# Performance work log

Measured on AMD Instinct MI355X. Metric: run time of the kernel, lower is better.

The kernel has to match this reference:

```python
import jax, jax.numpy as jnp
import numpy as np

HIDDEN = 1024
QDIM = 16
B, S = 4, 2048
EPS = 1e-8


def setup_inputs() -> dict:
    key = jax.random.key(0)
    ks = jax.random.split(key, 12)
    sc_h = 1.0 / np.sqrt(HIDDEN)
    inp = {
        "x": jax.random.normal(ks[0], (B, S, HIDDEN), dtype=jnp.float32),
        "Wq": jax.random.normal(ks[1], (HIDDEN, HIDDEN), dtype=jnp.float32) * sc_h,
        "bq": jnp.zeros((HIDDEN,), dtype=jnp.float32),
        "Wk": jax.random.normal(ks[2], (HIDDEN, HIDDEN), dtype=jnp.float32) * sc_h,
        "bk": jnp.zeros((HIDDEN,), dtype=jnp.float32),
        "Wv": jax.random.normal(ks[3], (HIDDEN, HIDDEN), dtype=jnp.float32) * sc_h,
        "bv": jnp.zeros((HIDDEN,), dtype=jnp.float32),
        "We": jax.random.normal(ks[4], (HIDDEN, QDIM), dtype=jnp.float32) * sc_h,
        "be": jnp.zeros((QDIM,), dtype=jnp.float32),
        "Wo": jax.random.normal(ks[5], (HIDDEN, HIDDEN), dtype=jnp.float32) * sc_h,
        "bo": jnp.zeros((HIDDEN,), dtype=jnp.float32),
    }
    return inp


def _quantum_embed(h, We, be):
    # Linear projection to quantum amplitude space, then normalize to a unit state.
    z = h @ We + be                     # [..., QDIM]
    nrm = jnp.sqrt(jnp.sum(z * z, axis=-1, keepdims=True) + EPS)
    return z / nrm


def reference(x, Wq, bq, Wk, bk, Wv, bv, We, be, Wo, bo):
    # Projections
    q = x @ Wq + bq                     # [B,S,H]
    k = x @ Wk + bk
    v = x @ Wv + bv
    # Quantum state embeddings (unit-normalized amplitudes)
    q_q = _quantum_embed(q, We, be)     # [B,S,QDIM]
    k_q = _quantum_embed(k, We, be)
    # Quantum fidelity similarity |<q|k>|^2, vectorized over all pairs
    ov = jnp.einsum("bqd,bkd->bqk", q_q, k_q)   # [B,S,S]
    attn = jax.nn.softmax(ov * ov, axis=-1)
    attended = jnp.einsum("bqk,bkh->bqh", attn, v)
    return attended @ Wo + bo
```

## Files before the change

### kernel.cpp

```cpp
#include <hip/hip_runtime.h>

#define H 1024
#define QD 16
#define BATCH 4
#define SEQ 2048
#define MROWS 8192
#define KCH 64

typedef __bf16 bf16x8 __attribute__((ext_vector_type(8)));
typedef __bf16 bf16x4 __attribute__((ext_vector_type(4)));
typedef float f32x4 __attribute__((ext_vector_type(4)));

__device__ __forceinline__ void async_g2l_16(const void* g, void* l) {
  __builtin_amdgcn_global_load_lds(
      (const __attribute__((address_space(1))) unsigned int*)g,
      (__attribute__((address_space(3))) unsigned int*)l, 16, 0, 0);
}

__global__ __launch_bounds__(256) void cvt_split(const float* __restrict__ src,
                                                 __bf16* __restrict__ hi,
                                                 __bf16* __restrict__ lo, int n) {
  int i = (blockIdx.x * 256 + threadIdx.x) * 4;
  if (i < n) {
    float4 f = *(const float4*)(src + i);
    bf16x4 h, l;
    h[0] = (__bf16)f.x; l[0] = (__bf16)(f.x - (float)h[0]);
    h[1] = (__bf16)f.y; l[1] = (__bf16)(f.y - (float)h[1]);
    h[2] = (__bf16)f.z; l[2] = (__bf16)(f.z - (float)h[2]);
    h[3] = (__bf16)f.w; l[3] = (__bf16)(f.w - (float)h[3]);
    *(bf16x4*)(hi + i) = h;
    *(bf16x4*)(lo + i) = l;
  }
}

__global__ __launch_bounds__(256) void transpose_cvt_f32_bf16(
    const float* __restrict__ src, __bf16* __restrict__ dst, int R, int C) {
  __shared__ float t[32][33];
  const int rb = blockIdx.y * 32, cb = blockIdx.x * 32;
  const int c = threadIdx.x & 31;
  const int r0 = threadIdx.x >> 5;
#pragma unroll
  for (int rr = r0; rr < 32; rr += 8)
    t[rr][c] = src[(long)(rb + rr) * C + cb + c];
  __syncthreads();
#pragma unroll
  for (int rr = r0; rr < 32; rr += 8)
    dst[(long)(cb + rr) * R + rb + c] = (__bf16)t[c][rr];
}

__global__ __launch_bounds__(256) void k2_cqk(const float* __restrict__ Wq,
                                              const float* __restrict__ Wk,
                                              const float* __restrict__ We,
                                              __bf16* __restrict__ Cth,
                                              __bf16* __restrict__ Ctl) {
  const int gw = blockIdx.x * 4 + (threadIdx.x >> 6);
  const int lane = threadIdx.x & 63;
  const int mat = gw & 1, k = gw >> 1;
  const float* Wrow = (mat ? Wk : Wq) + (long)k * H;
  const int col = lane & 15, q4 = lane >> 4;
  float acc = 0.f;
  for (int n0 = 0; n0 < 256; ++n0) {
    int n = q4 * 256 + n0;
    acc += Wrow[n] * We[n * QD + col];
  }
  acc += __shfl_xor(acc, 16);
  acc += __shfl_xor(acc, 32);
  if (lane < 16) {
    __bf16 hi = (__bf16)acc;
    __bf16 lo = (__bf16)(acc - (float)hi);
    long idx = (long)(mat * 16 + col) * H + k;
    Cth[idx] = hi;
    Ctl[idx] = lo;
  }
}

__global__ void k2b_dvec(const float* __restrict__ bq, const float* __restrict__ bk,
                         const float* __restrict__ We, const float* __restrict__ be,
                         float* __restrict__ dvec) {
  int j = threadIdx.x;
  if (j < 32) {
    int mat = j >> 4, col = j & 15;
    const float* b = mat ? bk : bq;
    float acc = be[col];
    for (int n = 0; n < H; ++n) acc += b[n] * We[n * QD + col];
    dvec[j] = acc;
  }
}

__global__ __launch_bounds__(256) void k3_embed_mfma(
    const __bf16* __restrict__ xh, const __bf16* __restrict__ xl,
    const __bf16* __restrict__ Cth, const __bf16* __restrict__ Ctl,
    const float* __restrict__ dvec, __bf16* __restrict__ qq32,
    __bf16* __restrict__ kk32) {
  __shared__ __bf16 Ah[32 * 64];
  __shared__ __bf16 Al[32 * 64];
  __shared__ __bf16 Bh[32 * 64];
  __shared__ __bf16 Bl[32 * 64];
  const int tid = threadIdx.x;
  const int lane = tid & 63;
  const int w = tid >> 6;
  const int rowhalf = w >> 1;
  const int ntile = w & 1;
  const int l15 = lane & 15, quad = lane >> 4;
  const long rowBase = (long)blockIdx.x * 32;

  const int srow = tid >> 3;
  const int segsw = ((tid & 7) ^ (srow & 7)) * 8;
  const __bf16* agh = xh + (rowBase + srow) * H + segsw;
  const __bf16* agl = xl + (rowBase + srow) * H + segsw;
  const __bf16* bgh = Cth + (long)srow * H + segsw;
  const __bf16* bgl = Ctl + (long)srow * H + segsw;
  __bf16* lah = &Ah[srow * 64 + (tid & 7) * 8];
  __bf16* lal = &Al[srow * 64 + (tid & 7) * 8];
  __bf16* lbh = &Bh[srow * 64 + (tid & 7) * 8];
  __bf16* lbl = &Bl[srow * 64 + (tid & 7) * 8];

  f32x4 acc;
  acc[0] = 0.f; acc[1] = 0.f; acc[2] = 0.f; acc[3] = 0.f;
  const int arow = (rowhalf * 16 + l15) * 64;
  const int brow = (ntile * 16 + l15) * 64;
  const int h7 = l15 & 7;

  for (int k0 = 0; k0 < H; k0 += 64) {
    async_g2l_16(agh + k0, lah);
    async_g2l_16(agl + k0, lal);
    async_g2l_16(bgh + k0, lbh);
    async_g2l_16(bgl + k0, lbl);
    __syncthreads();
#pragma unroll
    for (int s = 0; s < 2; ++s) {
      const int slot = ((s * 4 + quad) ^ h7) * 8;
      bf16x8 fah = *(const bf16x8*)&Ah[arow + slot];
      bf16x8 fal = *(const bf16x8*)&Al[arow + slot];
      bf16x8 fbh = *(const bf16x8*)&Bh[brow + slot];
      bf16x8 fbl = *(const bf16x8*)&Bl[brow + slot];
      acc = __builtin_amdgcn_mfma_f32_16x16x32_bf16(fah, fbh, acc, 0, 0, 0);
      acc = __builtin_amdgcn_mfma_f32_16x16x32_bf16(fal, fbh, acc, 0, 0, 0);
      acc = __builtin_amdgcn_mfma_f32_16x16x32_bf16(fah, fbl, acc, 0, 0, 0);
    }
    __syncthreads();
  }

  const float dv = dvec[ntile * 16 + l15];
  const float osc = ntile ? 1.0f : 1.20112240878f;
  __bf16* outp = ntile ? kk32 : qq32;
#pragma unroll
  for (int r = 0; r < 4; ++r) {
    float z = acc[r] + dv;
    float s2 = z * z;
    s2 += __shfl_xor(s2, 1);
    s2 += __shfl_xor(s2, 2);
    s2 += __shfl_xor(s2, 4);
    s2 += __shfl_xor(s2, 8);
    float val = z * rsqrtf(s2 + 1e-8f) * osc;
    long row = rowBase + rowhalf * 16 + quad * 4 + r;
    outp[row * 32 + l15] = (__bf16)val;
    outp[row * 32 + 16 + l15] = (__bf16)0.f;
  }
}

__global__ __launch_bounds__(512) void fused_attn(
    const __bf16* __restrict__ qq32, const __bf16* __restrict__ kk32,
    const __bf16* __restrict__ v_t, __bf16* __restrict__ attn) {
  __shared__ __bf16 Vlds[3][256 * KCH];
  __shared__ __bf16 Plds[2][128 * KCH];
  __shared__ float rsum2[128 * 2];
  const int tid = threadIdx.x;
  const int lane = tid & 63;
  const int w = tid >> 6;
  const int l15 = lane & 15, quad = lane >> 4;
  const int ws_k = w & 1, ws_q = w >> 1;
  const int wp_h = w & 3, wp_q = w >> 2;
  const int b = blockIdx.z;
  const long qbase = (long)blockIdx.x * 128;
  const long hbase = (long)blockIdx.y * 256;

  bf16x8 bq[2];
  {
    const __bf16* qqp =
        qq32 + ((long)b * SEQ + qbase + ws_q * 32 + l15) * 32 + quad * 8;
    bq[0] = *(const bf16x8*)qqp;
    bq[1] = *(const bf16x8*)(qqp + 16 * 32);
  }
  const __bf16* kkb = kk32 + ((long)b * SEQ + ws_k * 32 + l15) * 32 + quad * 8;

  const int vR = tid >> 3;
  const int vSL = (tid & 7) ^ (vR & 7);
  const __bf16* vgbase = v_t + (long)b * H * SEQ + (hbase + vR) * SEQ + vSL * 8;

  f32x4 acc[4][4];
#pragma unroll
  for (int i = 0; i < 4; ++i)
#pragma unroll
    for (int j = 0; j < 4; ++j) {
      acc[i][j][0] = 0.f; acc[i][j][1] = 0.f; acc[i][j][2] = 0.f; acc[i][j][3] = 0.f;
    }
  float rsPart[2] = {0.f, 0.f};

#pragma unroll
  for (int j = 0; j < 4; ++j)
    async_g2l_16(vgbase + (long)j * 64 * SEQ, &Vlds[0][j * 64 * KCH + tid * 8]);
  bf16x8 ak[2];
  ak[0] = *(const bf16x8*)kkb;
  ak[1] = *(const bf16x8*)(kkb + 16 * 32);

  int vcur = 0, vnxt = 1;
  for (int t = 0; t < SEQ / KCH; ++t) {
    const int kn = ((t + 1) & (SEQ / KCH - 1)) * KCH;
#pragma unroll
    for (int j = 0; j < 4; ++j)
      async_g2l_16(vgbase + (long)j * 64 * SEQ + kn,
                   &Vlds[vnxt][j * 64 * KCH + tid * 8]);

    __bf16* Pw = Plds[t & 1];
#pragma unroll
    for (int i = 0; i < 2; ++i) {
#pragma unroll
      for (int n = 0; n < 2; ++n) {
        f32x4 s;
        s[0] = 0.f; s[1] = 0.f; s[2] = 0.f; s[3] = 0.f;
        s = __builtin_amdgcn_mfma_f32_16x16x32_bf16(ak[i], bq[n], s, 0, 0, 0);
        bf16x4 pw;
        float part = 0.f;
#pragma unroll
        for (int r = 0; r < 4; ++r) {
          float wgt = exp2f(s[r] * s[r]);
          part += wgt;
          pw[r] = (__bf16)wgt;
        }
        rsPart[n] += part;
        const int q = ws_q * 32 + n * 16 + l15;
        const int g = ws_k * 4 + i * 2 + (quad >> 1);
        *(bf16x4*)&Pw[q * KCH + ((g ^ (q & 7)) << 3) + (quad & 1) * 4] = pw;
      }
    }
    ak[0] = *(const bf16x8*)(kkb + (long)kn * 32);
    ak[1] = *(const bf16x8*)(kkb + (long)(kn + 16) * 32);

    asm volatile("s_waitcnt lgkmcnt(0)" ::: "memory");
    asm volatile("s_waitcnt vmcnt(6)" ::: "memory");
    __builtin_amdgcn_sched_barrier(0);
    __builtin_amdgcn_s_barrier();

    const __bf16* Vr = Vlds[vcur];
#pragma unroll
    for (int ks = 0; ks < 2; ++ks) {
      bf16x8 ap[4], bv[4];
#pragma unroll
      for (int i = 0; i < 4; ++i) {
        const int q = wp_q * 64 + i * 16 + l15;
        ap[i] = *(const bf16x8*)&Pw[q * KCH + (((ks * 4 + quad) ^ (q & 7)) << 3)];
      }
#pragma unroll
      for (int j = 0; j < 4; ++j) {
        const int vr = wp_h * 64 + j * 16 + l15;
        bv[j] = *(const bf16x8*)&Vr[vr * KCH + (((ks * 4 + quad) ^ (vr & 7)) << 3)];
      }
#pragma unroll
      for (int i = 0; i < 4; ++i)
#pragma unroll
        for (int j = 0; j < 4; ++j)
          acc[i][j] =
              __builtin_amdgcn_mfma_f32_16x16x32_bf16(ap[i], bv[j], acc[i][j], 0, 0, 0);
    }
    const int third = 3 - vcur - vnxt;
    vcur = vnxt;
    vnxt = third;
  }

#pragma unroll
  for (int n = 0; n < 2; ++n) {
    float vs = rsPart[n];
    vs += __shfl_xor(vs, 16);
    vs += __shfl_xor(vs, 32);
    if (lane < 16) rsum2[(ws_q * 32 + n * 16 + l15) * 2 + ws_k] = vs;
  }
  __syncthreads();

  float rinv[4][4];
#pragma unroll
  for (int i = 0; i < 4; ++i)
#pragma unroll
    for (int r = 0; r < 4; ++r) {
      int row = wp_q * 64 + i * 16 + quad * 4 + r;
      rinv[i][r] = 1.0f / (rsum2[row * 2] + rsum2[row * 2 + 1]);
    }

  __bf16* ob = attn + ((long)b * SEQ + qbase) * H + hbase;
#pragma unroll
  for (int i = 0; i < 4; ++i)
#pragma unroll
    for (int j = 0; j < 4; ++j) {
      const int colL = wp_h * 64 + j * 16 + l15;
#pragma unroll
      for (int r = 0; r < 4; ++r) {
        const int rowL = wp_q * 64 + i * 16 + quad * 4 + r;
        ob[(long)rowL * H + colL] = (__bf16)(acc[i][j][r] * rinv[i][r]);
      }
    }
}

template <int OUTMODE, int HASBIAS>
__global__ __launch_bounds__(256) void gemm_bt(
    const __bf16* __restrict__ A, const __bf16* __restrict__ Bt,
    void* __restrict__ Cout, const float* __restrict__ bias, int M, int N, int K) {
  __shared__ __bf16 Alds[128 * 64];
  __shared__ __bf16 Blds[128 * 64];
  const int tid = threadIdx.x;
  const int lane = tid & 63;
  const int w = tid >> 6;
  const int wm = w >> 1, wn = w & 1;
  const int l15 = lane & 15, quad = lane >> 4;
  const long rowBase = (long)blockIdx.y * 128;
  const long colBase = (long)blockIdx.x * 128;

  const int srow = lane >> 3;
  const int segsw = ((lane & 7) ^ srow) * 8;

  const __bf16* ag[4];
  const __bf16* bg[4];
  __bf16* as_[4];
  __bf16* bs_[4];
#pragma unroll
  for (int j = 0; j < 4; ++j) {
    int r = j * 32 + w * 8;
    ag[j] = A + (rowBase + r + srow) * (long)K + segsw;
    bg[j] = Bt + (colBase + r + srow) * (long)K + segsw;
    as_[j] = &Alds[r * 64 + (lane & 7) * 8];
    bs_[j] = &Blds[r * 64 + (lane & 7) * 8];
  }

  f32x4 acc[4][4];
#pragma unroll
  for (int i = 0; i < 4; ++i)
#pragma unroll
    for (int j = 0; j < 4; ++j) {
      acc[i][j][0] = 0.f; acc[i][j][1] = 0.f; acc[i][j][2] = 0.f; acc[i][j][3] = 0.f;
    }

  const int h7 = l15 & 7;

  for (int k0 = 0; k0 < K; k0 += 64) {
#pragma unroll
    for (int j = 0; j < 4; ++j) {
      async_g2l_16(ag[j], as_[j]);
      async_g2l_16(bg[j], bs_[j]);
      ag[j] += 64;
      bg[j] += 64;
    }
    __syncthreads();
#pragma unroll
    for (int s = 0; s < 2; ++s) {
      const int slot = ((s * 4 + quad) ^ h7) * 8;
      bf16x8 af[4], bfv[4];
#pragma unroll
      for (int i = 0; i < 4; ++i) {
        af[i] = *(const bf16x8*)&Alds[(wm * 64 + i * 16 + l15) * 64 + slot];
        bfv[i] = *(const bf16x8*)&Blds[(wn * 64 + i * 16 + l15) * 64 + slot];
      }
#pragma unroll
      for (int i = 0; i < 4; ++i)
#pragma unroll
        for (int j = 0; j < 4; ++j)
          acc[i][j] =
              __builtin_amdgcn_mfma_f32_16x16x32_bf16(af[i], bfv[j], acc[i][j], 0, 0, 0);
    }
    __syncthreads();
  }

  const long crow0 = rowBase + wm * 64 + quad * 4;
  const long ccol0 = colBase + wn * 64 + l15;
#pragma unroll
  for (int i = 0; i < 4; ++i) {
#pragma unroll
    for (int j = 0; j < 4; ++j) {
      long col = ccol0 + j * 16;
      float bb = HASBIAS ? bias[col] : 0.f;
      if (OUTMODE == 2) {
        long row0 = crow0 + i * 16;
        int bz = (int)(row0 >> 11);
        long rb = row0 & (SEQ - 1);
        bf16x4 pv;
#pragma unroll
        for (int r = 0; r < 4; ++r) pv[r] = (__bf16)(acc[i][j][r] + bb);
        *(bf16x4*)&((__bf16*)Cout)[((long)bz * N + col) * SEQ + rb] = pv;
      } else {
#pragma unroll
        for (int r = 0; r < 4; ++r) {
          long row = crow0 + i * 16 + r;
          float val = acc[i][j][r] + bb;
          if (OUTMODE == 0)
            ((float*)Cout)[row * N + col] = val;
          else
            ((__bf16*)Cout)[row * N + col] = (__bf16)val;
        }
      }
    }
  }
}

extern "C" void kernel_launch(void* const* d_in, const int* in_sizes, int n_in,
                              void* d_out, int out_size, void* d_ws, size_t ws_size,
                              hipStream_t stream) {
  const float* x = (const float*)d_in[0];
  const float* Wq = (const float*)d_in[1];
  const float* bq = (const float*)d_in[2];
  const float* Wk = (const float*)d_in[3];
  const float* bk = (const float*)d_in[4];
  const float* Wv = (const float*)d_in[5];
  const float* bv = (const float*)d_in[6];
  const float* We = (const float*)d_in[7];
  const float* be = (const float*)d_in[8];
  const float* Wo = (const float*)d_in[9];
  const float* bo = (const float*)d_in[10];
  float* out = (float*)d_out;

  char* ws = (char*)d_ws;
  size_t o = 0;
  auto alloc = [&](size_t n) {
    size_t r = o;
    o += (n + 255) & ~(size_t)255;
    return r;
  };
  __bf16* xbf = (__bf16*)(ws + alloc((size_t)MROWS * H * 2));
  __bf16* v_t = (__bf16*)(ws + alloc((size_t)MROWS * H * 2));
  __bf16* attn = (__bf16*)(ws + alloc((size_t)MROWS * H * 2));
  __bf16* Wvt = (__bf16*)(ws + alloc((size_t)H * H * 2));
  __bf16* Wot = (__bf16*)(ws + alloc((size_t)H * H * 2));
  __bf16* Cth = (__bf16*)(ws + alloc((size_t)32 * H * 2));
  __bf16* Ctl = (__bf16*)(ws + alloc((size_t)32 * H * 2));
  float* dvec = (float*)(ws + alloc(32 * 4));
  __bf16* qq32 = (__bf16*)(ws + alloc((size_t)MROWS * 32 * 2));
  __bf16* kk32 = (__bf16*)(ws + alloc((size_t)MROWS * 32 * 2));
  __bf16* xlo = attn;
  if (ws_size < o) return;

  cvt_split<<<MROWS * H / 1024, 256, 0, stream>>>(x, xbf, xlo, MROWS * H);
  transpose_cvt_f32_bf16<<<dim3(32, 32), 256, 0, stream>>>(Wv, Wvt, H, H);
  transpose_cvt_f32_bf16<<<dim3(32, 32), 256, 0, stream>>>(Wo, Wot, H, H);
  k2_cqk<<<512, 256, 0, stream>>>(Wq, Wk, We, Cth, Ctl);
  k2b_dvec<<<1, 64, 0, stream>>>(bq, bk, We, be, dvec);
  k3_embed_mfma<<<MROWS / 32, 256, 0, stream>>>(xbf, xlo, Cth, Ctl, dvec, qq32, kk32);
  gemm_bt<2, 1><<<dim3(8, 64), 256, 0, stream>>>(xbf, Wvt, v_t, bv, MROWS, H, H);
  fused_attn<<<dim3(16, 4, BATCH), 512, 0, stream>>>(qq32, kk32, v_t, attn);
  gemm_bt<0, 1><<<dim3(8, 64), 256, 0, stream>>>(attn, Wot, out, bo, MROWS, H, H);
}
```

Baseline: 256.8 us.

## Split-K embed kernel, parallelize dvec, vectorize cqk, XCD-aware attention block mapping

The embedding MFMA kernel now uses 1024 threads per block, splitting the K=1024 reduction across four wave groups, with partial sums reduced through LDS. The bias-projection kernel spreads its reduction over 512 threads instead of 32, and the Wq/Wk·We kernel uses float4 loads with unrolling. The attention kernel switches to a flat 1D grid with a remap so that blocks sharing the same batch and head panel land on the same XCD, aiming for better L2 reuse of V. In exchange, the embed kernel uses more LDS and needs an extra barrier, and the block remap assumes round-robin dispatch across eight XCDs.

```diff
diff --git a/kernel.cpp b/kernel.cpp
--- a/kernel.cpp
+++ b/kernel.cpp
@@ -58,10 +58,16 @@
   const int mat = gw & 1, k = gw >> 1;
   const float* Wrow = (mat ? Wk : Wq) + (long)k * H;
   const int col = lane & 15, q4 = lane >> 4;
+  const float* wp = Wrow + q4 * 256;
+  const float* wep = We + (long)q4 * 256 * QD + col;
   float acc = 0.f;
-  for (int n0 = 0; n0 < 256; ++n0) {
-    int n = q4 * 256 + n0;
-    acc += Wrow[n] * We[n * QD + col];
+#pragma unroll 4
+  for (int n0 = 0; n0 < 256; n0 += 4) {
+    float4 w4 = *(const float4*)(wp + n0);
+    acc += w4.x * wep[(n0 + 0) * QD];
+    acc += w4.y * wep[(n0 + 1) * QD];
+    acc += w4.z * wep[(n0 + 2) * QD];
+    acc += w4.w * wep[(n0 + 3) * QD];
   }
   acc += __shfl_xor(acc, 16);
   acc += __shfl_xor(acc, 32);
@@ -74,46 +80,59 @@
   }
 }
 
-__global__ void k2b_dvec(const float* __restrict__ bq, const float* __restrict__ bk,
-                         const float* __restrict__ We, const float* __restrict__ be,
-                         float* __restrict__ dvec) {
-  int j = threadIdx.x;
-  if (j < 32) {
-    int mat = j >> 4, col = j & 15;
-    const float* b = mat ? bk : bq;
-    float acc = be[col];
-    for (int n = 0; n < H; ++n) acc += b[n] * We[n * QD + col];
-    dvec[j] = acc;
-  }
-}
-
-__global__ __launch_bounds__(256) void k3_embed_mfma(
+__global__ __launch_bounds__(512) void k2b_dvec(
+    const float* __restrict__ bq, const float* __restrict__ bk,
+    const float* __restrict__ We, const float* __restrict__ be,
+    float* __restrict__ dvec) {
+  __shared__ float part[16][32];
+  const int tid = threadIdx.x;
+  const int j = tid & 31, p = tid >> 5;
+  const int mat = j >> 4, col = j & 15;
+  const float* b = mat ? bk : bq;
+  float acc = 0.f;
+  for (int n = p * 64; n < p * 64 + 64; ++n) acc += b[n] * We[n * QD + col];
+  part[p][j] = acc;
+  __syncthreads();
+  if (tid < 32) {
+    float sum = be[tid & 15];
+    for (int p2 = 0; p2 < 16; ++p2) sum += part[p2][tid];
+    dvec[tid] = sum;
+  }
+}
+
+__global__ __launch_bounds__(1024) void k3_embed_mfma(
     const __bf16* __restrict__ xh, const __bf16* __restrict__ xl,
     const __bf16* __restrict__ Cth, const __bf16* __restrict__ Ctl,
     const float* __restrict__ dvec, __bf16* __restrict__ qq32,
     __bf16* __restrict__ kk32) {
-  __shared__ __bf16 Ah[32 * 64];
-  __shared__ __bf16 Al[32 * 64];
-  __shared__ __bf16 Bh[32 * 64];
-  __shared__ __bf16 Bl[32 * 64];
+  __shared__ __bf16 Ah[4][32 * 64];
+  __shared__ __bf16 Al[4][32 * 64];
+  __shared__ __bf16 Bh[4][32 * 64];
+  __shared__ __bf16 Bl[4][32 * 64];
   const int tid = threadIdx.x;
   const int lane = tid & 63;
   const int w = tid >> 6;
-  const int rowhalf = w >> 1;
-  const int ntile = w & 1;
+  const int kb = w >> 2;
+  const int w4 = w & 3;
+  const int rowhalf = w4 >> 1;
+  const int ntile = w4 & 1;
   const int l15 = lane & 15, quad = lane >> 4;
   const long rowBase = (long)blockIdx.x * 32;
 
-  const int srow = tid >> 3;
-  const int segsw = ((tid & 7) ^ (srow & 7)) * 8;
-  const __bf16* agh = xh + (rowBase + srow) * H + segsw;
-  const __bf16* agl = xl + (rowBase + srow) * H + segsw;
-  const __bf16* bgh = Cth + (long)srow * H + segsw;
-  const __bf16* bgl = Ctl + (long)srow * H + segsw;
-  __bf16* lah = &Ah[srow * 64 + (tid & 7) * 8];
-  __bf16* lal = &Al[srow * 64 + (tid & 7) * 8];
-  __bf16* lbh = &Bh[srow * 64 + (tid & 7) * 8];
-  __bf16* lbl = &Bl[srow * 64 + (tid & 7) * 8];
+  const int half = tid >> 8;
+  const int tl = tid & 255;
+  const int srow = tl >> 3;
+  const int seg = tl & 7;
+  const int segsw = (seg ^ (srow & 7)) * 8;
+  const long gk = half * 256 + segsw;
+  const __bf16* agh = xh + (rowBase + srow) * H + gk;
+  const __bf16* agl = xl + (rowBase + srow) * H + gk;
+  const __bf16* bgh = Cth + (long)srow * H + gk;
+  const __bf16* bgl = Ctl + (long)srow * H + gk;
+  __bf16* lah = &Ah[half][srow * 64 + seg * 8];
+  __bf16* lal = &Al[half][srow * 64 + seg * 8];
+  __bf16* lbh = &Bh[half][srow * 64 + seg * 8];
+  __bf16* lbl = &Bl[half][srow * 64 + seg * 8];
 
   f32x4 acc;
   acc[0] = 0.f; acc[1] = 0.f; acc[2] = 0.f; acc[3] = 0.f;
@@ -121,7 +140,7 @@
   const int brow = (ntile * 16 + l15) * 64;
   const int h7 = l15 & 7;
 
-  for (int k0 = 0; k0 < H; k0 += 64) {
+  for (int k0 = 0; k0 < 256; k0 += 64) {
     async_g2l_16(agh + k0, lah);
     async_g2l_16(agl + k0, lal);
     async_g2l_16(bgh + k0, lbh);
@@ -130,10 +149,10 @@
 #pragma unroll
     for (int s = 0; s < 2; ++s) {
       const int slot = ((s * 4 + quad) ^ h7) * 8;
-      bf16x8 fah = *(const bf16x8*)&Ah[arow + slot];
-      bf16x8 fal = *(const bf16x8*)&Al[arow + slot];
-      bf16x8 fbh = *(const bf16x8*)&Bh[brow + slot];
-      bf16x8 fbl = *(const bf16x8*)&Bl[brow + slot];
+      bf16x8 fah = *(const bf16x8*)&Ah[kb][arow + slot];
+      bf16x8 fal = *(const bf16x8*)&Al[kb][arow + slot];
+      bf16x8 fbh = *(const bf16x8*)&Bh[kb][brow + slot];
+      bf16x8 fbl = *(const bf16x8*)&Bl[kb][brow + slot];
       acc = __builtin_amdgcn_mfma_f32_16x16x32_bf16(fah, fbh, acc, 0, 0, 0);
       acc = __builtin_amdgcn_mfma_f32_16x16x32_bf16(fal, fbh, acc, 0, 0, 0);
       acc = __builtin_amdgcn_mfma_f32_16x16x32_bf16(fah, fbl, acc, 0, 0, 0);
@@ -141,21 +160,30 @@
     __syncthreads();
   }
 
-  const float dv = dvec[ntile * 16 + l15];
-  const float osc = ntile ? 1.0f : 1.20112240878f;
-  __bf16* outp = ntile ? kk32 : qq32;
-#pragma unroll
-  for (int r = 0; r < 4; ++r) {
-    float z = acc[r] + dv;
-    float s2 = z * z;
-    s2 += __shfl_xor(s2, 1);
-    s2 += __shfl_xor(s2, 2);
-    s2 += __shfl_xor(s2, 4);
-    s2 += __shfl_xor(s2, 8);
-    float val = z * rsqrtf(s2 + 1e-8f) * osc;
-    long row = rowBase + rowhalf * 16 + quad * 4 + r;
-    outp[row * 32 + l15] = (__bf16)val;
-    outp[row * 32 + 16 + l15] = (__bf16)0.f;
+  if (kb > 0) ((f32x4*)&Ah[kb][0])[w4 * 64 + lane] = acc;
+  __syncthreads();
+  if (kb == 0) {
+#pragma unroll
+    for (int q = 1; q < 4; ++q) {
+      f32x4 o = ((const f32x4*)&Ah[q][0])[w4 * 64 + lane];
+      acc[0] += o[0]; acc[1] += o[1]; acc[2] += o[2]; acc[3] += o[3];
+    }
+    const float dv = dvec[ntile * 16 + l15];
+    const float osc = ntile ? 1.0f : 1.20112240878f;
+    __bf16* outp = ntile ? kk32 : qq32;
+#pragma unroll
+    for (int r = 0; r < 4; ++r) {
+      float z = acc[r] + dv;
+      float s2 = z * z;
+      s2 += __shfl_xor(s2, 1);
+      s2 += __shfl_xor(s2, 2);
+      s2 += __shfl_xor(s2, 4);
+      s2 += __shfl_xor(s2, 8);
+      float val = z * rsqrtf(s2 + 1e-8f) * osc;
+      long row = rowBase + rowhalf * 16 + quad * 4 + r;
+      outp[row * 32 + l15] = (__bf16)val;
+      outp[row * 32 + 16 + l15] = (__bf16)0.f;
+    }
   }
 }
 
@@ -171,9 +199,13 @@
   const int l15 = lane & 15, quad = lane >> 4;
   const int ws_k = w & 1, ws_q = w >> 1;
   const int wp_h = w & 3, wp_q = w >> 2;
-  const int b = blockIdx.z;
-  const long qbase = (long)blockIdx.x * 128;
-  const long hbase = (long)blockIdx.y * 256;
+
+  const int bid = blockIdx.x;
+  const int xcd = bid & 7, s = bid >> 3;
+  const int panel = xcd * 2 + (s >> 4);
+  const int b = panel >> 2;
+  const long hbase = (long)(panel & 3) * 256;
+  const long qbase = (long)(s & 15) * 128;
 
   bf16x8 bq[2];
   {
@@ -217,14 +249,14 @@
     for (int i = 0; i < 2; ++i) {
 #pragma unroll
       for (int n = 0; n < 2; ++n) {
-        f32x4 s;
-        s[0] = 0.f; s[1] = 0.f; s[2] = 0.f; s[3] = 0.f;
-        s = __builtin_amdgcn_mfma_f32_16x16x32_bf16(ak[i], bq[n], s, 0, 0, 0);
+        f32x4 s2v;
+        s2v[0] = 0.f; s2v[1] = 0.f; s2v[2] = 0.f; s2v[3] = 0.f;
+        s2v = __builtin_amdgcn_mfma_f32_16x16x32_bf16(ak[i], bq[n], s2v, 0, 0, 0);
         bf16x4 pw;
         float part = 0.f;
 #pragma unroll
         for (int r = 0; r < 4; ++r) {
-          float wgt = exp2f(s[r] * s[r]);
+          float wgt = exp2f(s2v[r] * s2v[r]);
           part += wgt;
           pw[r] = (__bf16)wgt;
         }
@@ -439,9 +471,9 @@
   transpose_cvt_f32_bf16<<<dim3(32, 32), 256, 0, stream>>>(Wv, Wvt, H, H);
   transpose_cvt_f32_bf16<<<dim3(32, 32), 256, 0, stream>>>(Wo, Wot, H, H);
   k2_cqk<<<512, 256, 0, stream>>>(Wq, Wk, We, Cth, Ctl);
-  k2b_dvec<<<1, 64, 0, stream>>>(bq, bk, We, be, dvec);
-  k3_embed_mfma<<<MROWS / 32, 256, 0, stream>>>(xbf, xlo, Cth, Ctl, dvec, qq32, kk32);
+  k2b_dvec<<<1, 512, 0, stream>>>(bq, bk, We, be, dvec);
+  k3_embed_mfma<<<MROWS / 32, 1024, 0, stream>>>(xbf, xlo, Cth, Ctl, dvec, qq32, kk32);
   gemm_bt<2, 1><<<dim3(8, 64), 256, 0, stream>>>(xbf, Wvt, v_t, bv, MROWS, H, H);
-  fused_attn<<<dim3(16, 4, BATCH), 512, 0, stream>>>(qq32, kk32, v_t, attn);
+  fused_attn<<<256, 512, 0, stream>>>(qq32, kk32, v_t, attn);
   gemm_bt<0, 1><<<dim3(8, 64), 256, 0, stream>>>(attn, Wot, out, bo, MROWS, H, H);
 }
```

Result: faster. 240.5 us (-6.4%).
